# Kernel tuning notes

Hardware: AMD Instinct MI355X
Metric: run time of the kernel (lower is better)

## Reference

```python
import jax, jax.numpy as jnp
import numpy as np

KH, KW, STRIDE, PAD, DIL = 3, 3, 1, 1, 1


def setup_inputs() -> dict:
    key = jax.random.key(0)
    ks = jax.random.split(key, 4)
    B, C, H, W, O = 4, 256, 64, 64, 256
    K = KH * KW
    x = jax.random.normal(ks[0], (B, C, H, W), jnp.float32)
    # offset/mask conv params (original inits to zero; use small random so offsets are non-trivial)
    w_om = jax.random.normal(ks[1], (3 * K, C, KH, KW), jnp.float32) * 0.01
    b_om = jnp.zeros((3 * K,), jnp.float32)
    # main weight: kaiming_uniform_(a=1) -> gain = sqrt(2/(1+1^2)) = 1, bound = sqrt(3)/sqrt(fan_in)
    fan_in = C * K
    bound = float(np.sqrt(3.0) / np.sqrt(fan_in))
    weight = jax.random.uniform(ks[2], (O, C, KH, KW), jnp.float32, -bound, bound)
    bias = jnp.zeros((O,), jnp.float32)
    return {"x": x, "w_om": w_om, "b_om": b_om, "weight": weight, "bias": bias}


def _deform_conv2d(x, offset, mask, weight, bias):
    # torchvision.ops.deform_conv2d semantics, deformable_groups=1, stride=1, pad=1, dil=1
    B, C, H, W = x.shape
    K = KH * KW
    # torchvision offset layout: per-tap interleaved (y, x) pairs along channel dim
    off_y = offset[:, 0::2]  # [B, K, H, W]
    off_x = offset[:, 1::2]  # [B, K, H, W]
    ky = (jnp.repeat(jnp.arange(KH), KW) * DIL).astype(x.dtype)  # [K]
    kx = (jnp.tile(jnp.arange(KW), KH) * DIL).astype(x.dtype)    # [K]
    base_y = (jnp.arange(H) * STRIDE - PAD).astype(x.dtype)
    base_x = (jnp.arange(W) * STRIDE - PAD).astype(x.dtype)
    py = base_y[None, None, :, None] + ky[None, :, None, None] + off_y  # [B,K,H,W]
    px = base_x[None, None, None, :] + kx[None, :, None, None] + off_x  # [B,K,H,W]
    y0 = jnp.floor(py)
    x0 = jnp.floor(px)
    ly = py - y0
    lx = px - x0
    y0i = y0.astype(jnp.int32)
    x0i = x0.astype(jnp.int32)
    x_flat = x.reshape(B, C, H * W)

    def gather(yy, xx):
        # zero-padded gather of one bilinear corner -> [B, C, K, H, W]
        valid = ((yy >= 0) & (yy < H) & (xx >= 0) & (xx < W)).astype(x.dtype)
        idx = (jnp.clip(yy, 0, H - 1) * W + jnp.clip(xx, 0, W - 1)).reshape(B, -1)
        g = jax.vmap(lambda xf, i: jnp.take(xf, i, axis=1))(x_flat, idx)
        return g.reshape(B, C, K, H, W) * valid.reshape(B, 1, K, H, W)

    w00 = ((1 - ly) * (1 - lx))[:, None]
    w01 = ((1 - ly) * lx)[:, None]
    w10 = (ly * (1 - lx))[:, None]
    w11 = (ly * lx)[:, None]
    val = (gather(y0i, x0i) * w00 + gather(y0i, x0i + 1) * w01
           + gather(y0i + 1, x0i) * w10 + gather(y0i + 1, x0i + 1) * w11)
    cols = val * mask[:, None]  # modulated columns [B,C,K,H,W]
    out = jnp.einsum('bckhw,ock->bohw', cols, weight.reshape(weight.shape[0], C, K))
    return out + bias[None, :, None, None]


def reference(x, w_om, b_om, weight, bias):
    om = jax.lax.conv_general_dilated(
        x, w_om, (STRIDE, STRIDE), ((PAD, PAD), (PAD, PAD)),
        rhs_dilation=(DIL, DIL), dimension_numbers=('NCHW', 'OIHW', 'NCHW'),
    ) + b_om[None, :, None, None]
    K = KH * KW
    o1, o2, m = om[:, :K], om[:, K:2 * K], om[:, 2 * K:]
    offset = jnp.concatenate([o1, o2], axis=1)  # [B, 2K, H, W]
    mask = jax.nn.sigmoid(m)                    # [B, K, H, W]
    return _deform_conv2d(x, offset, mask, weight, bias)
```

## Files before the change

kernel.cpp:

```cpp
#include <hip/hip_runtime.h>
#include <stdint.h>

#define B_ 4
#define C_ 256
#define H_ 64
#define W_ 64
#define O_ 256
#define K_ 9
#define CK 2304
#define HW 4096
#define NTOT 16384

typedef __bf16 bf16x8 __attribute__((ext_vector_type(8)));
typedef __bf16 bf16x4 __attribute__((ext_vector_type(4)));
typedef float f32x4 __attribute__((ext_vector_type(4)));
typedef float f32x2 __attribute__((ext_vector_type(2)));
typedef f32x2 __attribute__((aligned(4))) f32x2u;

__device__ __forceinline__ uint16_t f2bf(float f) {
  uint32_t u = __builtin_bit_cast(uint32_t, f);
  return (uint16_t)((u + 0x7FFFu + ((u >> 16) & 1u)) >> 16);
}

__device__ __forceinline__ uint32_t pk_bf16(float a, float b) {
  uint16_t lo = __builtin_bit_cast(uint16_t, (__bf16)a);
  uint16_t hi = __builtin_bit_cast(uint16_t, (__bf16)b);
  return (uint32_t)lo | ((uint32_t)hi << 16);
}

__global__ void k0_wconv(const float* __restrict__ weight, uint16_t* __restrict__ wb) {
  int idx = blockIdx.x * 256 + threadIdx.x;
  if (idx >= O_ * CK) return;
  int o = idx / CK;
  int rem = idx - o * CK;
  int k = rem >> 8;
  int c = rem & 255;
  wb[idx] = f2bf(weight[(o * C_ + c) * K_ + k]);
}

__global__ void k0b_womb(const float* __restrict__ w_om, uint16_t* __restrict__ womb) {
  int idx = blockIdx.x * 256 + threadIdx.x;
  if (idx >= 32 * CK) return;
  int j = idx / CK;
  int ck = idx - j * CK;
  int k = ck >> 8, c = ck & 255;
  womb[idx] = (j < 27) ? f2bf(w_om[(j * 256 + c) * 9 + k]) : (uint16_t)0;
}

__global__ void k2a_xT(const float* __restrict__ x, uint16_t* __restrict__ xT) {
  int bx = blockIdx.x;
  int ct = bx & 3;
  int hwt = (bx >> 2) & 63;
  int b = bx >> 8;
  int t = threadIdx.x;
  int l = t & 63;
  int cq = t >> 6;

  __shared__ __align__(16) uint16_t tile[64 * 72];

  const float* xb = x + ((b * 256 + ct * 64) * HW) + hwt * 64;
#pragma unroll
  for (int i = 0; i < 16; ++i) {
    int c = cq * 16 + i;
    tile[l * 72 + c] = f2bf(xb[c * HW + l]);
  }
  __syncthreads();

  int hw = t >> 2;
  int c8 = (t & 3) * 8;
  uint16_t* dst = xT + ((size_t)b << 20) + (size_t)(hwt * 64 + hw) * 256 + ct * 64;
  *(uint4*)&dst[c8] = *(const uint4*)&tile[hw * 72 + c8];
  *(uint4*)&dst[c8 + 32] = *(const uint4*)&tile[hw * 72 + c8 + 32];
}

__global__ void k1_mfma(const uint16_t* __restrict__ womb, const uint16_t* __restrict__ xT,
                        float* __restrict__ ompart) {
  int bx = blockIdx.x;
  int ks = bx >> 8;
  int nt = bx & 255;
  int t = threadIdx.x;
  int lane = t & 63;
  int wid = t >> 6;
  int lr = lane & 15, q = lane >> 4;
  int n = nt * 64 + wid * 16 + lr;
  int b = n >> 12;
  int hw = n & 4095;
  int y = hw >> 6, xx = hw & 63;
  const uint16_t* xb = xT + ((size_t)b << 20);
  const uint16_t* zrow = womb + 31 * CK;

  f32x4 acc0 = {0.f, 0.f, 0.f, 0.f};
  f32x4 acc1 = {0.f, 0.f, 0.f, 0.f};

  for (int kk = 0; kk < 3; ++kk) {
    int k = ks * 3 + kk;
    int dy = k / 3, dx = k - dy * 3;
    int ny = y + dy - 1, nx = xx + dx - 1;
    bool valid = ((unsigned)ny < 64u) && ((unsigned)nx < 64u);
    int row = (min(max(ny, 0), 63) << 6) + min(max(nx, 0), 63);
    const uint16_t* bp = valid ? (xb + row * 256 + q * 8) : (zrow + q * 8);
    const uint16_t* ap = womb + lr * CK + k * 256 + q * 8;
#pragma unroll
    for (int kt = 0; kt < 8; ++kt) {
      int c0 = kt * 32;
      bf16x8 bF = *(const bf16x8*)&bp[c0];
      bf16x8 aF0 = *(const bf16x8*)&ap[c0];
      bf16x8 aF1 = *(const bf16x8*)&ap[16 * CK + c0];
      acc0 = __builtin_amdgcn_mfma_f32_16x16x32_bf16(aF0, bF, acc0, 0, 0, 0);
      acc1 = __builtin_amdgcn_mfma_f32_16x16x32_bf16(aF1, bF, acc1, 0, 0, 0);
    }
  }

  float* op = ompart + ks * (32 * NTOT);
#pragma unroll
  for (int r = 0; r < 4; ++r) {
    op[(q * 4 + r) * NTOT + n] = acc0[r];
    op[(16 + q * 4 + r) * NTOT + n] = acc1[r];
  }
}

__global__ void k1b_ppm(const float* __restrict__ ompart, const float* __restrict__ b_om,
                        float* __restrict__ pypxmk) {
  int tid = blockIdx.x * 256 + threadIdx.x;
  int k = tid >> 14;
  int n = tid & 16383;
  int b = n >> 12;
  int hw = n & 4095;
  int h = hw >> 6, w = hw & 63;
  const float* p0 = ompart;
  const float* p1 = ompart + 32 * NTOT;
  const float* p2 = ompart + 64 * NTOT;
  int iy = (2 * k) * NTOT + n;
  int ix = (2 * k + 1) * NTOT + n;
  int im = (18 + k) * NTOT + n;
  float oy = p0[iy] + p1[iy] + p2[iy] + b_om[2 * k];
  float ox = p0[ix] + p1[ix] + p2[ix] + b_om[2 * k + 1];
  float m = p0[im] + p1[im] + p2[im] + b_om[18 + k];
  int off = (b * 9 + k) * HW + hw;
  pypxmk[off] = (float)(h - 1 + k / 3) + oy;
  pypxmk[147456 + off] = (float)(w - 1 + k % 3) + ox;
  pypxmk[294912 + off] = 1.f / (1.f + __expf(-m));
}

__global__ void k1_offconv(const float* __restrict__ x, const float* __restrict__ w_om,
                           const float* __restrict__ b_om, float* __restrict__ pypxmk) {
  int bx = blockIdx.x;
  int jq = bx % 7;
  int h = (bx / 7) % H_;
  int b = bx / (7 * H_);
  int t = threadIdx.x;
  int w = t & 63;
  int cs = __builtin_amdgcn_readfirstlane(t >> 6);

  float acc[4] = {0.f, 0.f, 0.f, 0.f};
  const float* xb = x + (b * C_) * HW;

  for (int ci = 0; ci < 64; ++ci) {
    int c = cs * 64 + ci;
    const float* xr = xb + c * HW;
    float xv[3][3];
#pragma unroll
    for (int r = 0; r < 3; ++r) {
      int y = h - 1 + r;
      bool yv = ((unsigned)y < 64u);
#pragma unroll
      for (int dx = 0; dx < 3; ++dx) {
        int xx = w - 1 + dx;
        bool v = yv && ((unsigned)xx < 64u);
        xv[r][dx] = v ? xr[y * 64 + xx] : 0.f;
      }
    }
    const float* wp = w_om + ((jq * 4) * C_ + c) * 9;
#pragma unroll
    for (int jj = 0; jj < 4; ++jj) {
      int j = jq * 4 + jj;
      int jeff = (j < 27) ? jj : 0;
      const float* wj = wp + jeff * (C_ * 9);
      float a = 0.f;
#pragma unroll
      for (int r = 0; r < 3; ++r)
#pragma unroll
        for (int dx = 0; dx < 3; ++dx)
          a = fmaf(xv[r][dx], wj[r * 3 + dx], a);
      acc[jj] += a;
    }
  }

  __shared__ float red[4][4][64];
#pragma unroll
  for (int jj = 0; jj < 4; ++jj) red[cs][jj][w] = acc[jj];
  __syncthreads();

  int jj = t >> 6;
  int j = jq * 4 + jj;
  if (j < 27) {
    float s = red[0][jj][w] + red[1][jj][w] + red[2][jj][w] + red[3][jj][w] + b_om[j];
    float* pyA = pypxmk;
    float* pxA = pypxmk + 147456;
    float* mkA = pypxmk + 294912;
    if (j < 18) {
      int k = j >> 1;
      int off = (b * 9 + k) * HW + h * 64 + w;
      if ((j & 1) == 0)
        pyA[off] = (float)(h - 1 + k / 3) + s;
      else
        pxA[off] = (float)(w - 1 + k % 3) + s;
    } else {
      int k = j - 18;
      mkA[(b * 9 + k) * HW + h * 64 + w] = 1.f / (1.f + __expf(-s));
    }
  }
}

__global__ void k2_cols(const uint16_t* __restrict__ xT, const float* __restrict__ pypxmk,
                        uint16_t* __restrict__ cols) {
  int bx = blockIdx.x;
  int g = __builtin_amdgcn_readfirstlane(threadIdx.x >> 6);
  int lane = threadIdx.x & 63;

  const float* pyA = pypxmk;
  const float* pxA = pypxmk + 147456;
  const float* mkA = pypxmk + 294912;

  for (int it = 0; it < 18; ++it) {
    int p = it * 4 + g;
    int pn = p / 9;
    int k = p - pn * 9;
    int n = (bx << 3) + pn;
    int b = n >> 12;
    int hw = n & 4095;
    int poff = (b * 9 + k) * HW + hw;
    float py = pyA[poff];
    float px = pxA[poff];
    float mk = mkA[poff];

    float fy0 = floorf(py), fx0 = floorf(px);
    float ly = py - fy0, lx = px - fx0;
    int y0 = (int)fy0, x0 = (int)fx0;
    bool vy0 = ((unsigned)y0 < 64u), vy1 = ((unsigned)(y0 + 1) < 64u);
    bool vx0 = ((unsigned)x0 < 64u), vx1 = ((unsigned)(x0 + 1) < 64u);
    float w00 = (vy0 && vx0) ? (1.f - ly) * (1.f - lx) * mk : 0.f;
    float w01 = (vy0 && vx1) ? (1.f - ly) * lx * mk : 0.f;
    float w10 = (vy1 && vx0) ? ly * (1.f - lx) * mk : 0.f;
    float w11 = (vy1 && vx1) ? ly * lx * mk : 0.f;
    bool sel0 = (x0 >= 63);
    bool sel1 = (x0 >= 0);
    float wa0 = (sel0 ? 0.f : w00) + (sel1 ? 0.f : w01);
    float wb0 = (sel0 ? w00 : 0.f) + (sel1 ? w01 : 0.f);
    float wa1 = (sel0 ? 0.f : w10) + (sel1 ? 0.f : w11);
    float wb1 = (sel0 ? w10 : 0.f) + (sel1 ? w11 : 0.f);
    int bx0 = min(max(x0, 0), 62);
    int a0 = min(max(y0, 0), 63) * 64 + bx0;
    int a1 = min(max(y0 + 1, 0), 63) * 64 + bx0;

    const uint16_t* xb = xT + ((size_t)b << 20);
    bf16x4 r00 = *(const bf16x4*)&xb[a0 * 256 + lane * 4];
    bf16x4 r01 = *(const bf16x4*)&xb[a0 * 256 + 256 + lane * 4];
    bf16x4 r10 = *(const bf16x4*)&xb[a1 * 256 + lane * 4];
    bf16x4 r11 = *(const bf16x4*)&xb[a1 * 256 + 256 + lane * 4];

    float v[4];
#pragma unroll
    for (int i = 0; i < 4; ++i)
      v[i] = wa0 * (float)r00[i] + wb0 * (float)r01[i] +
             wa1 * (float)r10[i] + wb1 * (float)r11[i];

    uint2 pk;
    pk.x = pk_bf16(v[0], v[1]);
    pk.y = pk_bf16(v[2], v[3]);
    *(uint2*)&cols[(size_t)n * CK + k * 256 + lane * 4] = pk;
  }
}

__global__ void k2_fb(const float* __restrict__ x, const float* __restrict__ pypxmk,
                      uint16_t* __restrict__ cols) {
  int bx = blockIdx.x;
  int cg = bx & 15;
  int h = (bx >> 4) & 63;
  int b = bx >> 10;
  int t = threadIdx.x;
  int w = t & 63;
  int g = t >> 6;

  const float* pyA = pypxmk;
  const float* pxA = pypxmk + 147456;
  const float* mkA = pypxmk + 294912;

  __shared__ uint16_t tile[64 * 146];
  const float* xb = x + b * C_ * HW;
  int cbase = cg * 16 + g * 4;

#pragma unroll
  for (int k = 0; k < 9; ++k) {
    int poff = (b * 9 + k) * HW + h * 64 + w;
    float py = pyA[poff];
    float px = pxA[poff];
    float mk = mkA[poff];
    float fy0 = floorf(py), fx0 = floorf(px);
    float ly = py - fy0, lx = px - fx0;
    int y0 = (int)fy0, x0 = (int)fx0;
    bool vy0 = ((unsigned)y0 < 64u), vy1 = ((unsigned)(y0 + 1) < 64u);
    bool vx0 = ((unsigned)x0 < 64u), vx1 = ((unsigned)(x0 + 1) < 64u);
    float w00 = (vy0 && vx0) ? (1.f - ly) * (1.f - lx) * mk : 0.f;
    float w01 = (vy0 && vx1) ? (1.f - ly) * lx * mk : 0.f;
    float w10 = (vy1 && vx0) ? ly * (1.f - lx) * mk : 0.f;
    float w11 = (vy1 && vx1) ? ly * lx * mk : 0.f;
    bool sel0 = (x0 >= 63);
    bool sel1 = (x0 >= 0);
    float wa0 = (sel0 ? 0.f : w00) + (sel1 ? 0.f : w01);
    float wb0 = (sel0 ? w00 : 0.f) + (sel1 ? w01 : 0.f);
    float wa1 = (sel0 ? 0.f : w10) + (sel1 ? 0.f : w11);
    float wb1 = (sel0 ? w10 : 0.f) + (sel1 ? w11 : 0.f);
    int bx0 = min(max(x0, 0), 62);
    int a0 = min(max(y0, 0), 63) * 64 + bx0;
    int a1 = min(max(y0 + 1, 0), 63) * 64 + bx0;

#pragma unroll
    for (int cp = 0; cp < 2; ++cp) {
      const float* xcA = xb + (cbase + cp * 2) * HW;
      const float* xcB = xcA + HW;
      f32x2 A0 = *(const f32x2u*)&xcA[a0];
      f32x2 A1 = *(const f32x2u*)&xcA[a1];
      f32x2 B0 = *(const f32x2u*)&xcB[a0];
      f32x2 B1 = *(const f32x2u*)&xcB[a1];
      float rA = wa0 * A0.x + wb0 * A0.y + wa1 * A1.x + wb1 * A1.y;
      float rB = wa0 * B0.x + wb0 * B0.y + wa1 * B1.x + wb1 * B1.y;
      *(uint32_t*)&tile[w * 146 + k * 16 + g * 4 + cp * 2] = pk_bf16(rA, rB);
    }
  }
  __syncthreads();

#pragma unroll
  for (int it = 0; it < 18; ++it) {
    int u = t + it * 256;
    int wu = u / 72;
    int rem = u - wu * 72;
    int k = rem >> 3;
    int cd = rem & 7;
    uint32_t val = *(const uint32_t*)&tile[wu * 146 + rem * 2];
    int n = b * HW + h * 64 + wu;
    int dst = n * CK + k * 256 + cg * 16 + cd * 2;
    *(uint32_t*)&cols[dst] = val;
  }
}

__global__ void k3_gemm(const uint16_t* __restrict__ wb, const uint16_t* __restrict__ cols,
                        const float* __restrict__ bias, float* __restrict__ dst,
                        int ktn, int withBias) {
  int bx = blockIdx.x;
  int ks = bx >> 8;
  int bxx = bx & 255;
  int mt = bxx & 1;
  int nt = bxx >> 1;
  int o0 = mt * 128;
  int n0 = nt * 128;
  int t = threadIdx.x;
  int lane = t & 63;
  int wid = t >> 6;
  int wm = wid >> 1, wn = wid & 1;
  int lr = lane & 15, q = lane >> 4;

  __shared__ __align__(16) uint16_t As[128 * 32];
  __shared__ __align__(16) uint16_t Bs[128 * 32];

  f32x4 acc[4][4];
  const f32x4 zero = {0.f, 0.f, 0.f, 0.f};
#pragma unroll
  for (int i = 0; i < 4; ++i)
#pragma unroll
    for (int j = 0; j < 4; ++j) acc[i][j] = zero;

  int r0 = t >> 2;
  int koff = (t & 3) * 8;
  int kb = ks * ktn * 32;
  const uint16_t* gA = wb + (o0 + r0) * CK + kb + koff;
  const uint16_t* gB = cols + (n0 + r0) * CK + kb + koff;

  for (int kt = 0; kt < ktn; ++kt) {
    int k0 = kt * 32;
    __builtin_amdgcn_global_load_lds(
        (const __attribute__((address_space(1))) uint32_t*)(gA + k0),
        (__attribute__((address_space(3))) uint32_t*)&As[t * 8], 16, 0, 0);
    __builtin_amdgcn_global_load_lds(
        (const __attribute__((address_space(1))) uint32_t*)(gA + 64 * CK + k0),
        (__attribute__((address_space(3))) uint32_t*)&As[2048 + t * 8], 16, 0, 0);
    __builtin_amdgcn_global_load_lds(
        (const __attribute__((address_space(1))) uint32_t*)(gB + k0),
        (__attribute__((address_space(3))) uint32_t*)&Bs[t * 8], 16, 0, 0);
    __builtin_amdgcn_global_load_lds(
        (const __attribute__((address_space(1))) uint32_t*)(gB + 64 * CK + k0),
        (__attribute__((address_space(3))) uint32_t*)&Bs[2048 + t * 8], 16, 0, 0);
    __syncthreads();

    bf16x8 aF[4], bF[4];
#pragma unroll
    for (int i = 0; i < 4; ++i)
      aF[i] = *(const bf16x8*)&As[(wm * 64 + i * 16 + lr) * 32 + q * 8];
#pragma unroll
    for (int j = 0; j < 4; ++j)
      bF[j] = *(const bf16x8*)&Bs[(wn * 64 + j * 16 + lr) * 32 + q * 8];
#pragma unroll
    for (int i = 0; i < 4; ++i)
#pragma unroll
      for (int j = 0; j < 4; ++j)
        acc[i][j] = __builtin_amdgcn_mfma_f32_16x16x32_bf16(aF[i], bF[j], acc[i][j], 0, 0, 0);
    __syncthreads();
  }

  float* base = dst + ks * (O_ * NTOT);
  int bb = n0 >> 12;
  int hw0 = n0 & 4095;
#pragma unroll
  for (int i = 0; i < 4; ++i) {
#pragma unroll
    for (int r = 0; r < 4; ++r) {
      int o = o0 + wm * 64 + i * 16 + q * 4 + r;
      float bv = withBias ? bias[o] : 0.f;
      float* orow = base + (bb * O_ + o) * HW + hw0;
#pragma unroll
      for (int j = 0; j < 4; ++j) orow[wn * 64 + j * 16 + lr] = acc[i][j][r] + bv;
    }
  }
}

__global__ void k4_reduce(const float* __restrict__ part, const float* __restrict__ bias,
                          float* __restrict__ out) {
  int i4 = blockIdx.x * 256 + threadIdx.x;
  const f32x4* p0 = (const f32x4*)part;
  const f32x4* p1 = p0 + (O_ * NTOT / 4);
  const f32x4* p2 = p1 + (O_ * NTOT / 4);
  f32x4 a = p0[i4] + p1[i4] + p2[i4];
  int o = (i4 >> 10) & 255;
  ((f32x4*)out)[i4] = a + bias[o];
}

extern "C" void kernel_launch(void* const* d_in, const int* in_sizes, int n_in,
                              void* d_out, int out_size, void* d_ws, size_t ws_size,
                              hipStream_t stream) {
  const float* x = (const float*)d_in[0];
  const float* w_om = (const float*)d_in[1];
  const float* b_om = (const float*)d_in[2];
  const float* weight = (const float*)d_in[3];
  const float* bias = (const float*)d_in[4];
  float* out = (float*)d_out;

  char* ws = (char*)d_ws;
  float* pypxmk = (float*)ws;
  uint16_t* wb = (uint16_t*)(ws + 1769472);
  uint16_t* cols = (uint16_t*)(ws + 2949120);
  uint16_t* xT = (uint16_t*)(ws + 78446592);
  uint16_t* womb = (uint16_t*)(ws + 86835200);
  float* ompart = (float*)(ws + 86982656);
  float* part = (float*)(ws + 93274112);

  bool xtpath = ws_size >= 86835200ull;
  bool mfmak1 = ws_size >= 93274112ull;
  bool splitk = ws_size >= 143605760ull;

  hipLaunchKernelGGL(k0_wconv, dim3(2304), dim3(256), 0, stream, weight, wb);

  if (xtpath) hipLaunchKernelGGL(k2a_xT, dim3(1024), dim3(256), 0, stream, x, xT);

  if (xtpath && mfmak1) {
    hipLaunchKernelGGL(k0b_womb, dim3(288), dim3(256), 0, stream, w_om, womb);
    hipLaunchKernelGGL(k1_mfma, dim3(768), dim3(256), 0, stream, womb, xT, ompart);
    hipLaunchKernelGGL(k1b_ppm, dim3(576), dim3(256), 0, stream, ompart, b_om, pypxmk);
  } else {
    hipLaunchKernelGGL(k1_offconv, dim3(4 * 64 * 7), dim3(256), 0, stream, x, w_om, b_om, pypxmk);
  }

  if (xtpath) {
    hipLaunchKernelGGL(k2_cols, dim3(2048), dim3(256), 0, stream, xT, pypxmk, cols);
  } else {
    hipLaunchKernelGGL(k2_fb, dim3(4 * 64 * 16), dim3(256), 0, stream, x, pypxmk, cols);
  }

  if (splitk) {
    hipLaunchKernelGGL(k3_gemm, dim3(768), dim3(256), 0, stream, wb, cols, bias, part, 24, 0);
    hipLaunchKernelGGL(k4_reduce, dim3(4096), dim3(256), 0, stream, part, bias, out);
  } else {
    hipLaunchKernelGGL(k3_gemm, dim3(256), dim3(256), 0, stream, wb, cols, bias, out, 72, 1);
  }
}
```

Baseline: 180.4 us.

## Merge prep kernels, fuse offset-conv epilogue, prefetch sampling params in cols

Three preprocessing kernels (weight conversion, offset-weight conversion, x transpose) become one launch that dispatches on block index. The offset MFMA kernel now covers all 9 taps without split-K and applies bias, sigmoid and position math in its epilogue, so the partial buffer and the reduce kernel are gone. In the cols kernel, the next iteration's py/px/mask loads are issued one iteration early so their latency overlaps the current gather. The aim is fewer launches and less intermediate traffic, at the cost of the offset GEMM using only 256 blocks and a rearranged workspace layout.

New measurement: 173.6 us. 3.8% less time.

```diff
diff --git a/kernel.cpp b/kernel.cpp
--- a/kernel.cpp
+++ b/kernel.cpp
@@ -28,56 +28,71 @@
   return (uint32_t)lo | ((uint32_t)hi << 16);
 }
 
-__global__ void k0_wconv(const float* __restrict__ weight, uint16_t* __restrict__ wb) {
-  int idx = blockIdx.x * 256 + threadIdx.x;
-  if (idx >= O_ * CK) return;
-  int o = idx / CK;
-  int rem = idx - o * CK;
-  int k = rem >> 8;
-  int c = rem & 255;
-  wb[idx] = f2bf(weight[(o * C_ + c) * K_ + k]);
-}
-
-__global__ void k0b_womb(const float* __restrict__ w_om, uint16_t* __restrict__ womb) {
-  int idx = blockIdx.x * 256 + threadIdx.x;
-  if (idx >= 32 * CK) return;
-  int j = idx / CK;
-  int ck = idx - j * CK;
-  int k = ck >> 8, c = ck & 255;
-  womb[idx] = (j < 27) ? f2bf(w_om[(j * 256 + c) * 9 + k]) : (uint16_t)0;
-}
-
-__global__ void k2a_xT(const float* __restrict__ x, uint16_t* __restrict__ xT) {
+__global__ void kA_prep(const float* __restrict__ weight, const float* __restrict__ w_om,
+                        const float* __restrict__ x, uint16_t* __restrict__ wb,
+                        uint16_t* __restrict__ womb, uint16_t* __restrict__ xT) {
   int bx = blockIdx.x;
-  int ct = bx & 3;
-  int hwt = (bx >> 2) & 63;
-  int b = bx >> 8;
   int t = threadIdx.x;
-  int l = t & 63;
-  int cq = t >> 6;
-
-  __shared__ __align__(16) uint16_t tile[64 * 72];
-
-  const float* xb = x + ((b * 256 + ct * 64) * HW) + hwt * 64;
-#pragma unroll
-  for (int i = 0; i < 16; ++i) {
-    int c = cq * 16 + i;
-    tile[l * 72 + c] = f2bf(xb[c * HW + l]);
-  }
-  __syncthreads();
-
-  int hw = t >> 2;
-  int c8 = (t & 3) * 8;
-  uint16_t* dst = xT + ((size_t)b << 20) + (size_t)(hwt * 64 + hw) * 256 + ct * 64;
-  *(uint4*)&dst[c8] = *(const uint4*)&tile[hw * 72 + c8];
-  *(uint4*)&dst[c8 + 32] = *(const uint4*)&tile[hw * 72 + c8 + 32];
+  if (bx < 2304) {
+    int idx = bx * 256 + t;
+    int o = idx / CK;
+    int rem = idx - o * CK;
+    int k = rem >> 8, c = rem & 255;
+    wb[idx] = f2bf(weight[(o * C_ + c) * K_ + k]);
+  } else if (bx < 2592) {
+    int idx = (bx - 2304) * 256 + t;
+    int j = idx / CK;
+    int ck = idx - j * CK;
+    int k = ck >> 8, c = ck & 255;
+    womb[idx] = (j < 27) ? f2bf(w_om[(j * 256 + c) * 9 + k]) : (uint16_t)0;
+  } else {
+    int bxl = bx - 2592;
+    int ct = bxl & 3;
+    int hwt = (bxl >> 2) & 63;
+    int b = bxl >> 8;
+    int l = t & 63;
+    int cq = t >> 6;
+
+    __shared__ __align__(16) uint16_t tile[64 * 72];
+
+    const float* xb = x + ((b * 256 + ct * 64) * HW) + hwt * 64;
+#pragma unroll
+    for (int i = 0; i < 16; ++i) {
+      int c = cq * 16 + i;
+      tile[l * 72 + c] = f2bf(xb[c * HW + l]);
+    }
+    __syncthreads();
+
+    int hw = t >> 2;
+    int c8 = (t & 3) * 8;
+    uint16_t* dst = xT + ((size_t)b << 20) + (size_t)(hwt * 64 + hw) * 256 + ct * 64;
+    *(uint4*)&dst[c8] = *(const uint4*)&tile[hw * 72 + c8];
+    *(uint4*)&dst[c8 + 32] = *(const uint4*)&tile[hw * 72 + c8 + 32];
+  }
+}
+
+__device__ __forceinline__ void write_om(float v, int j, int n, const float* __restrict__ b_om,
+                                         float* __restrict__ pypxmk) {
+  if (j >= 27) return;
+  float s = v + b_om[j];
+  int b = n >> 12, hw = n & 4095;
+  int h = hw >> 6, w = hw & 63;
+  if (j < 18) {
+    int k = j >> 1;
+    int off = (b * 9 + k) * HW + hw;
+    if ((j & 1) == 0)
+      pypxmk[off] = (float)(h - 1 + k / 3) + s;
+    else
+      pypxmk[147456 + off] = (float)(w - 1 + k % 3) + s;
+  } else {
+    int k = j - 18;
+    pypxmk[294912 + (b * 9 + k) * HW + hw] = 1.f / (1.f + __expf(-s));
+  }
 }
 
 __global__ void k1_mfma(const uint16_t* __restrict__ womb, const uint16_t* __restrict__ xT,
-                        float* __restrict__ ompart) {
-  int bx = blockIdx.x;
-  int ks = bx >> 8;
-  int nt = bx & 255;
+                        const float* __restrict__ b_om, float* __restrict__ pypxmk) {
+  int nt = blockIdx.x;
   int t = threadIdx.x;
   int lane = t & 63;
   int wid = t >> 6;
@@ -92,8 +107,8 @@
   f32x4 acc0 = {0.f, 0.f, 0.f, 0.f};
   f32x4 acc1 = {0.f, 0.f, 0.f, 0.f};
 
-  for (int kk = 0; kk < 3; ++kk) {
-    int k = ks * 3 + kk;
+#pragma unroll
+  for (int k = 0; k < 9; ++k) {
     int dy = k / 3, dx = k - dy * 3;
     int ny = y + dy - 1, nx = xx + dx - 1;
     bool valid = ((unsigned)ny < 64u) && ((unsigned)nx < 64u);
@@ -111,104 +126,10 @@
     }
   }
 
-  float* op = ompart + ks * (32 * NTOT);
 #pragma unroll
   for (int r = 0; r < 4; ++r) {
-    op[(q * 4 + r) * NTOT + n] = acc0[r];
-    op[(16 + q * 4 + r) * NTOT + n] = acc1[r];
-  }
-}
-
-__global__ void k1b_ppm(const float* __restrict__ ompart, const float* __restrict__ b_om,
-                        float* __restrict__ pypxmk) {
-  int tid = blockIdx.x * 256 + threadIdx.x;
-  int k = tid >> 14;
-  int n = tid & 16383;
-  int b = n >> 12;
-  int hw = n & 4095;
-  int h = hw >> 6, w = hw & 63;
-  const float* p0 = ompart;
-  const float* p1 = ompart + 32 * NTOT;
-  const float* p2 = ompart + 64 * NTOT;
-  int iy = (2 * k) * NTOT + n;
-  int ix = (2 * k + 1) * NTOT + n;
-  int im = (18 + k) * NTOT + n;
-  float oy = p0[iy] + p1[iy] + p2[iy] + b_om[2 * k];
-  float ox = p0[ix] + p1[ix] + p2[ix] + b_om[2 * k + 1];
-  float m = p0[im] + p1[im] + p2[im] + b_om[18 + k];
-  int off = (b * 9 + k) * HW + hw;
-  pypxmk[off] = (float)(h - 1 + k / 3) + oy;
-  pypxmk[147456 + off] = (float)(w - 1 + k % 3) + ox;
-  pypxmk[294912 + off] = 1.f / (1.f + __expf(-m));
-}
-
-__global__ void k1_offconv(const float* __restrict__ x, const float* __restrict__ w_om,
-                           const float* __restrict__ b_om, float* __restrict__ pypxmk) {
-  int bx = blockIdx.x;
-  int jq = bx % 7;
-  int h = (bx / 7) % H_;
-  int b = bx / (7 * H_);
-  int t = threadIdx.x;
-  int w = t & 63;
-  int cs = __builtin_amdgcn_readfirstlane(t >> 6);
-
-  float acc[4] = {0.f, 0.f, 0.f, 0.f};
-  const float* xb = x + (b * C_) * HW;
-
-  for (int ci = 0; ci < 64; ++ci) {
-    int c = cs * 64 + ci;
-    const float* xr = xb + c * HW;
-    float xv[3][3];
-#pragma unroll
-    for (int r = 0; r < 3; ++r) {
-      int y = h - 1 + r;
-      bool yv = ((unsigned)y < 64u);
-#pragma unroll
-      for (int dx = 0; dx < 3; ++dx) {
-        int xx = w - 1 + dx;
-        bool v = yv && ((unsigned)xx < 64u);
-        xv[r][dx] = v ? xr[y * 64 + xx] : 0.f;
-      }
-    }
-    const float* wp = w_om + ((jq * 4) * C_ + c) * 9;
-#pragma unroll
-    for (int jj = 0; jj < 4; ++jj) {
-      int j = jq * 4 + jj;
-      int jeff = (j < 27) ? jj : 0;
-      const float* wj = wp + jeff * (C_ * 9);
-      float a = 0.f;
-#pragma unroll
-      for (int r = 0; r < 3; ++r)
-#pragma unroll
-        for (int dx = 0; dx < 3; ++dx)
-          a = fmaf(xv[r][dx], wj[r * 3 + dx], a);
-      acc[jj] += a;
-    }
-  }
-
-  __shared__ float red[4][4][64];
-#pragma unroll
-  for (int jj = 0; jj < 4; ++jj) red[cs][jj][w] = acc[jj];
-  __syncthreads();
-
-  int jj = t >> 6;
-  int j = jq * 4 + jj;
-  if (j < 27) {
-    float s = red[0][jj][w] + red[1][jj][w] + red[2][jj][w] + red[3][jj][w] + b_om[j];
-    float* pyA = pypxmk;
-    float* pxA = pypxmk + 147456;
-    float* mkA = pypxmk + 294912;
-    if (j < 18) {
-      int k = j >> 1;
-      int off = (b * 9 + k) * HW + h * 64 + w;
-      if ((j & 1) == 0)
-        pyA[off] = (float)(h - 1 + k / 3) + s;
-      else
-        pxA[off] = (float)(w - 1 + k % 3) + s;
-    } else {
-      int k = j - 18;
-      mkA[(b * 9 + k) * HW + h * 64 + w] = 1.f / (1.f + __expf(-s));
-    }
+    write_om(acc0[r], q * 4 + r, n, b_om, pypxmk);
+    write_om(acc1[r], 16 + q * 4 + r, n, b_om, pypxmk);
   }
 }
 
@@ -221,6 +142,18 @@
   const float* pyA = pypxmk;
   const float* pxA = pypxmk + 147456;
   const float* mkA = pypxmk + 294912;
+
+  float py_c, px_c, mk_c;
+  {
+    int p = g;
+    int pn = p / 9;
+    int k = p - pn * 9;
+    int n = (bx << 3) + pn;
+    int poff = ((n >> 12) * 9 + k) * HW + (n & 4095);
+    py_c = pyA[poff];
+    px_c = pxA[poff];
+    mk_c = mkA[poff];
+  }
 
   for (int it = 0; it < 18; ++it) {
     int p = it * 4 + g;
@@ -228,11 +161,18 @@
     int k = p - pn * 9;
     int n = (bx << 3) + pn;
     int b = n >> 12;
-    int hw = n & 4095;
-    int poff = (b * 9 + k) * HW + hw;
-    float py = pyA[poff];
-    float px = pxA[poff];
-    float mk = mkA[poff];
+
+    float py = py_c, px = px_c, mk = mk_c;
+    if (it < 17) {
+      int p2 = (it + 1) * 4 + g;
+      int pn2 = p2 / 9;
+      int k2 = p2 - pn2 * 9;
+      int n2 = (bx << 3) + pn2;
+      int poff2 = ((n2 >> 12) * 9 + k2) * HW + (n2 & 4095);
+      py_c = pyA[poff2];
+      px_c = pxA[poff2];
+      mk_c = mkA[poff2];
+    }
 
     float fy0 = floorf(py), fx0 = floorf(px);
     float ly = py - fy0, lx = px - fx0;
@@ -269,6 +209,176 @@
     pk.x = pk_bf16(v[0], v[1]);
     pk.y = pk_bf16(v[2], v[3]);
     *(uint2*)&cols[(size_t)n * CK + k * 256 + lane * 4] = pk;
+  }
+}
+
+__global__ void k3_gemm(const uint16_t* __restrict__ wb, const uint16_t* __restrict__ cols,
+                        const float* __restrict__ bias, float* __restrict__ dst,
+                        int ktn, int withBias) {
+  int bx = blockIdx.x;
+  int ks = bx >> 8;
+  int bxx = bx & 255;
+  int mt = bxx & 1;
+  int nt = bxx >> 1;
+  int o0 = mt * 128;
+  int n0 = nt * 128;
+  int t = threadIdx.x;
+  int lane = t & 63;
+  int wid = t >> 6;
+  int wm = wid >> 1, wn = wid & 1;
+  int lr = lane & 15, q = lane >> 4;
+
+  __shared__ __align__(16) uint16_t As[128 * 32];
+  __shared__ __align__(16) uint16_t Bs[128 * 32];
+
+  f32x4 acc[4][4];
+  const f32x4 zero = {0.f, 0.f, 0.f, 0.f};
+#pragma unroll
+  for (int i = 0; i < 4; ++i)
+#pragma unroll
+    for (int j = 0; j < 4; ++j) acc[i][j] = zero;
+
+  int r0 = t >> 2;
+  int koff = (t & 3) * 8;
+  int kb = ks * ktn * 32;
+  const uint16_t* gA = wb + (o0 + r0) * CK + kb + koff;
+  const uint16_t* gB = cols + (n0 + r0) * CK + kb + koff;
+
+  for (int kt = 0; kt < ktn; ++kt) {
+    int k0 = kt * 32;
+    __builtin_amdgcn_global_load_lds(
+        (const __attribute__((address_space(1))) uint32_t*)(gA + k0),
+        (__attribute__((address_space(3))) uint32_t*)&As[t * 8], 16, 0, 0);
+    __builtin_amdgcn_global_load_lds(
+        (const __attribute__((address_space(1))) uint32_t*)(gA + 64 * CK + k0),
+        (__attribute__((address_space(3))) uint32_t*)&As[2048 + t * 8], 16, 0, 0);
+    __builtin_amdgcn_global_load_lds(
+        (const __attribute__((address_space(1))) uint32_t*)(gB + k0),
+        (__attribute__((address_space(3))) uint32_t*)&Bs[t * 8], 16, 0, 0);
+    __builtin_amdgcn_global_load_lds(
+        (const __attribute__((address_space(1))) uint32_t*)(gB + 64 * CK + k0),
+        (__attribute__((address_space(3))) uint32_t*)&Bs[2048 + t * 8], 16, 0, 0);
+    __syncthreads();
+
+    bf16x8 aF[4], bF[4];
+#pragma unroll
+    for (int i = 0; i < 4; ++i)
+      aF[i] = *(const bf16x8*)&As[(wm * 64 + i * 16 + lr) * 32 + q * 8];
+#pragma unroll
+    for (int j = 0; j < 4; ++j)
+      bF[j] = *(const bf16x8*)&Bs[(wn * 64 + j * 16 + lr) * 32 + q * 8];
+#pragma unroll
+    for (int i = 0; i < 4; ++i)
+#pragma unroll
+      for (int j = 0; j < 4; ++j)
+        acc[i][j] = __builtin_amdgcn_mfma_f32_16x16x32_bf16(aF[i], bF[j], acc[i][j], 0, 0, 0);
+    __syncthreads();
+  }
+
+  float* base = dst + ks * (O_ * NTOT);
+  int bb = n0 >> 12;
+  int hw0 = n0 & 4095;
+#pragma unroll
+  for (int i = 0; i < 4; ++i) {
+#pragma unroll
+    for (int r = 0; r < 4; ++r) {
+      int o = o0 + wm * 64 + i * 16 + q * 4 + r;
+      float bv = withBias ? bias[o] : 0.f;
+      float* orow = base + (bb * O_ + o) * HW + hw0;
+#pragma unroll
+      for (int j = 0; j < 4; ++j) orow[wn * 64 + j * 16 + lr] = acc[i][j][r] + bv;
+    }
+  }
+}
+
+__global__ void k4_reduce(const float* __restrict__ part, const float* __restrict__ bias,
+                          float* __restrict__ out) {
+  int i4 = blockIdx.x * 256 + threadIdx.x;
+  const f32x4* p0 = (const f32x4*)part;
+  const f32x4* p1 = p0 + (O_ * NTOT / 4);
+  const f32x4* p2 = p1 + (O_ * NTOT / 4);
+  f32x4 a = p0[i4] + p1[i4] + p2[i4];
+  int o = (i4 >> 10) & 255;
+  ((f32x4*)out)[i4] = a + bias[o];
+}
+
+__global__ void k0_wconv(const float* __restrict__ weight, uint16_t* __restrict__ wb) {
+  int idx = blockIdx.x * 256 + threadIdx.x;
+  if (idx >= O_ * CK) return;
+  int o = idx / CK;
+  int rem = idx - o * CK;
+  int k = rem >> 8;
+  int c = rem & 255;
+  wb[idx] = f2bf(weight[(o * C_ + c) * K_ + k]);
+}
+
+__global__ void k1_offconv(const float* __restrict__ x, const float* __restrict__ w_om,
+                           const float* __restrict__ b_om, float* __restrict__ pypxmk) {
+  int bx = blockIdx.x;
+  int jq = bx % 7;
+  int h = (bx / 7) % H_;
+  int b = bx / (7 * H_);
+  int t = threadIdx.x;
+  int w = t & 63;
+  int cs = __builtin_amdgcn_readfirstlane(t >> 6);
+
+  float acc[4] = {0.f, 0.f, 0.f, 0.f};
+  const float* xb = x + (b * C_) * HW;
+
+  for (int ci = 0; ci < 64; ++ci) {
+    int c = cs * 64 + ci;
+    const float* xr = xb + c * HW;
+    float xv[3][3];
+#pragma unroll
+    for (int r = 0; r < 3; ++r) {
+      int y = h - 1 + r;
+      bool yv = ((unsigned)y < 64u);
+#pragma unroll
+      for (int dx = 0; dx < 3; ++dx) {
+        int xx = w - 1 + dx;
+        bool v = yv && ((unsigned)xx < 64u);
+        xv[r][dx] = v ? xr[y * 64 + xx] : 0.f;
+      }
+    }
+    const float* wp = w_om + ((jq * 4) * C_ + c) * 9;
+#pragma unroll
+    for (int jj = 0; jj < 4; ++jj) {
+      int j = jq * 4 + jj;
+      int jeff = (j < 27) ? jj : 0;
+      const float* wj = wp + jeff * (C_ * 9);
+      float a = 0.f;
+#pragma unroll
+      for (int r = 0; r < 3; ++r)
+#pragma unroll
+        for (int dx = 0; dx < 3; ++dx)
+          a = fmaf(xv[r][dx], wj[r * 3 + dx], a);
+      acc[jj] += a;
+    }
+  }
+
+  __shared__ float red[4][4][64];
+#pragma unroll
+  for (int jj = 0; jj < 4; ++jj) red[cs][jj][w] = acc[jj];
+  __syncthreads();
+
+  int jj = t >> 6;
+  int j = jq * 4 + jj;
+  if (j < 27) {
+    float s = red[0][jj][w] + red[1][jj][w] + red[2][jj][w] + red[3][jj][w] + b_om[j];
+    float* pyA = pypxmk;
+    float* pxA = pypxmk + 147456;
+    float* mkA = pypxmk + 294912;
+    if (j < 18) {
+      int k = j >> 1;
+      int off = (b * 9 + k) * HW + h * 64 + w;
+      if ((j & 1) == 0)
+        pyA[off] = (float)(h - 1 + k / 3) + s;
+      else
+        pxA[off] = (float)(w - 1 + k % 3) + s;
+    } else {
+      int k = j - 18;
+      mkA[(b * 9 + k) * HW + h * 64 + w] = 1.f / (1.f + __expf(-s));
+    }
   }
 }
 
@@ -344,96 +454,6 @@
   }
 }
 
-__global__ void k3_gemm(const uint16_t* __restrict__ wb, const uint16_t* __restrict__ cols,
-                        const float* __restrict__ bias, float* __restrict__ dst,
-                        int ktn, int withBias) {
-  int bx = blockIdx.x;
-  int ks = bx >> 8;
-  int bxx = bx & 255;
-  int mt = bxx & 1;
-  int nt = bxx >> 1;
-  int o0 = mt * 128;
-  int n0 = nt * 128;
-  int t = threadIdx.x;
-  int lane = t & 63;
-  int wid = t >> 6;
-  int wm = wid >> 1, wn = wid & 1;
-  int lr = lane & 15, q = lane >> 4;
-
-  __shared__ __align__(16) uint16_t As[128 * 32];
-  __shared__ __align__(16) uint16_t Bs[128 * 32];
-
-  f32x4 acc[4][4];
-  const f32x4 zero = {0.f, 0.f, 0.f, 0.f};
-#pragma unroll
-  for (int i = 0; i < 4; ++i)
-#pragma unroll
-    for (int j = 0; j < 4; ++j) acc[i][j] = zero;
-
-  int r0 = t >> 2;
-  int koff = (t & 3) * 8;
-  int kb = ks * ktn * 32;
-  const uint16_t* gA = wb + (o0 + r0) * CK + kb + koff;
-  const uint16_t* gB = cols + (n0 + r0) * CK + kb + koff;
-
-  for (int kt = 0; kt < ktn; ++kt) {
-    int k0 = kt * 32;
-    __builtin_amdgcn_global_load_lds(
-        (const __attribute__((address_space(1))) uint32_t*)(gA + k0),
-        (__attribute__((address_space(3))) uint32_t*)&As[t * 8], 16, 0, 0);
-    __builtin_amdgcn_global_load_lds(
-        (const __attribute__((address_space(1))) uint32_t*)(gA + 64 * CK + k0),
-        (__attribute__((address_space(3))) uint32_t*)&As[2048 + t * 8], 16, 0, 0);
-    __builtin_amdgcn_global_load_lds(
-        (const __attribute__((address_space(1))) uint32_t*)(gB + k0),
-        (__attribute__((address_space(3))) uint32_t*)&Bs[t * 8], 16, 0, 0);
-    __builtin_amdgcn_global_load_lds(
-        (const __attribute__((address_space(1))) uint32_t*)(gB + 64 * CK + k0),
-        (__attribute__((address_space(3))) uint32_t*)&Bs[2048 + t * 8], 16, 0, 0);
-    __syncthreads();
-
-    bf16x8 aF[4], bF[4];
-#pragma unroll
-    for (int i = 0; i < 4; ++i)
-      aF[i] = *(const bf16x8*)&As[(wm * 64 + i * 16 + lr) * 32 + q * 8];
-#pragma unroll
-    for (int j = 0; j < 4; ++j)
-      bF[j] = *(const bf16x8*)&Bs[(wn * 64 + j * 16 + lr) * 32 + q * 8];
-#pragma unroll
-    for (int i = 0; i < 4; ++i)
-#pragma unroll
-      for (int j = 0; j < 4; ++j)
-        acc[i][j] = __builtin_amdgcn_mfma_f32_16x16x32_bf16(aF[i], bF[j], acc[i][j], 0, 0, 0);
-    __syncthreads();
-  }
-
-  float* base = dst + ks * (O_ * NTOT);
-  int bb = n0 >> 12;
-  int hw0 = n0 & 4095;
-#pragma unroll
-  for (int i = 0; i < 4; ++i) {
-#pragma unroll
-    for (int r = 0; r < 4; ++r) {
-      int o = o0 + wm * 64 + i * 16 + q * 4 + r;
-      float bv = withBias ? bias[o] : 0.f;
-      float* orow = base + (bb * O_ + o) * HW + hw0;
-#pragma unroll
-      for (int j = 0; j < 4; ++j) orow[wn * 64 + j * 16 + lr] = acc[i][j][r] + bv;
-    }
-  }
-}
-
-__global__ void k4_reduce(const float* __restrict__ part, const float* __restrict__ bias,
-                          float* __restrict__ out) {
-  int i4 = blockIdx.x * 256 + threadIdx.x;
-  const f32x4* p0 = (const f32x4*)part;
-  const f32x4* p1 = p0 + (O_ * NTOT / 4);
-  const f32x4* p2 = p1 + (O_ * NTOT / 4);
-  f32x4 a = p0[i4] + p1[i4] + p2[i4];
-  int o = (i4 >> 10) & 255;
-  ((f32x4*)out)[i4] = a + bias[o];
-}
-
 extern "C" void kernel_launch(void* const* d_in, const int* in_sizes, int n_in,
                               void* d_out, int out_size, void* d_ws, size_t ws_size,
                               hipStream_t stream) {
@@ -445,40 +465,25 @@
   float* out = (float*)d_out;
 
   char* ws = (char*)d_ws;
-  float* pypxmk = (float*)ws;
-  uint16_t* wb = (uint16_t*)(ws + 1769472);
-  uint16_t* cols = (uint16_t*)(ws + 2949120);
-  uint16_t* xT = (uint16_t*)(ws + 78446592);
-  uint16_t* womb = (uint16_t*)(ws + 86835200);
-  float* ompart = (float*)(ws + 86982656);
-  float* part = (float*)(ws + 93274112);
-
-  bool xtpath = ws_size >= 86835200ull;
-  bool mfmak1 = ws_size >= 93274112ull;
-  bool splitk = ws_size >= 143605760ull;
-
-  hipLaunchKernelGGL(k0_wconv, dim3(2304), dim3(256), 0, stream, weight, wb);
-
-  if (xtpath) hipLaunchKernelGGL(k2a_xT, dim3(1024), dim3(256), 0, stream, x, xT);
-
-  if (xtpath && mfmak1) {
-    hipLaunchKernelGGL(k0b_womb, dim3(288), dim3(256), 0, stream, w_om, womb);
-    hipLaunchKernelGGL(k1_mfma, dim3(768), dim3(256), 0, stream, womb, xT, ompart);
-    hipLaunchKernelGGL(k1b_ppm, dim3(576), dim3(256), 0, stream, ompart, b_om, pypxmk);
-  } else {
-    hipLaunchKernelGGL(k1_offconv, dim3(4 * 64 * 7), dim3(256), 0, stream, x, w_om, b_om, pypxmk);
-  }
-
-  if (xtpath) {
+  uint16_t* wb = (uint16_t*)ws;
+  uint16_t* womb = (uint16_t*)(ws + 1179648);
+  uint16_t* xT = (uint16_t*)(ws + 1327104);
+  float* pypxmk = (float*)(ws + 9715712);
+  uint16_t* cols = (uint16_t*)(ws + 11485184);
+  float* part = (float*)(ws + 86982656);
+
+  if (ws_size >= 137314304ull) {
+    hipLaunchKernelGGL(kA_prep, dim3(3616), dim3(256), 0, stream, weight, w_om, x, wb, womb, xT);
+    hipLaunchKernelGGL(k1_mfma, dim3(256), dim3(256), 0, stream, womb, xT, b_om, pypxmk);
     hipLaunchKernelGGL(k2_cols, dim3(2048), dim3(256), 0, stream, xT, pypxmk, cols);
-  } else {
-    hipLaunchKernelGGL(k2_fb, dim3(4 * 64 * 16), dim3(256), 0, stream, x, pypxmk, cols);
-  }
-
-  if (splitk) {
     hipLaunchKernelGGL(k3_gemm, dim3(768), dim3(256), 0, stream, wb, cols, bias, part, 24, 0);
     hipLaunchKernelGGL(k4_reduce, dim3(4096), dim3(256), 0, stream, part, bias, out);
   } else {
-    hipLaunchKernelGGL(k3_gemm, dim3(256), dim3(256), 0, stream, wb, cols, bias, out, 72, 1);
-  }
-}
+    float* pypx_fb = (float*)(ws + 1179648);
+    uint16_t* colsf = (uint16_t*)(ws + 2949120);
+    hipLaunchKernelGGL(k0_wconv, dim3(2304), dim3(256), 0, stream, weight, wb);
+    hipLaunchKernelGGL(k1_offconv, dim3(4 * 64 * 7), dim3(256), 0, stream, x, w_om, b_om, pypx_fb);
+    hipLaunchKernelGGL(k2_fb, dim3(4 * 64 * 16), dim3(256), 0, stream, x, pypx_fb, colsf);
+    hipLaunchKernelGGL(k3_gemm, dim3(256), dim3(256), 0, stream, wb, colsf, bias, out, 72, 1);
+  }
+}
```
